# Kernel tuning notes

Measured on AMD Instinct MI355X. Metric: run time of the kernel, lower is better.

Reference implementation:

```python
import jax, jax.numpy as jnp
import numpy as np

B, T, NX, NXS, H, NY, NYS = 16384, 60, 4, 3, 64, 4, 3


def _lstm(x, h0, c0, Wih, Whh, bih, bhh):
    """PyTorch-convention LSTM (gate order i,f,g,o). x: [B,T,X]. Returns (hs [B,T,H], hT, cT)."""
    # precompute input contribution for all timesteps: [T,B,4H]
    xg = jnp.transpose(jnp.einsum('btx,gx->btg', x, Wih) + (bih + bhh), (1, 0, 2))

    def step(carry, xg_t):
        h, c = carry
        g = xg_t + h @ Whh.T
        i, f, gg, o = jnp.split(g, 4, axis=-1)
        c = jax.nn.sigmoid(f) * c + jax.nn.sigmoid(i) * jnp.tanh(gg)
        h = jax.nn.sigmoid(o) * jnp.tanh(c)
        return (h, c), h

    (hT, cT), hs = jax.lax.scan(step, (h0, c0), xg)
    return jnp.transpose(hs, (1, 0, 2)), hT, cT


def setup_inputs() -> dict:
    key = jax.random.key(0)
    ks = jax.random.split(key, 24)
    w = lambda k, shp: (jax.random.normal(k, shp, jnp.float32) * 0.1)
    return {
        'inputs_main': jax.random.normal(ks[0], (B, T, NX), jnp.float32),
        'inputs_aux': jax.random.normal(ks[1], (B, NXS), jnp.float32),
        'hx2': jax.random.normal(ks[2], (B, H), jnp.float32),
        'cx2': jax.random.normal(ks[3], (B, H), jnp.float32),
        'Ws1': w(ks[4], (H, NXS)), 'bs1': w(ks[5], (H,)),
        'Ws2': w(ks[6], (H, NXS)), 'bs2': w(ks[7], (H,)),
        'Wih1': w(ks[8], (4 * H, NX)), 'Whh1': w(ks[9], (4 * H, H)),
        'bih1': w(ks[10], (4 * H,)), 'bhh1': w(ks[11], (4 * H,)),
        'Wih2': w(ks[12], (4 * H, H)), 'Whh2': w(ks[13], (4 * H, H)),
        'bih2': w(ks[14], (4 * H,)), 'bhh2': w(ks[15], (4 * H,)),
        'Wlat': w(ks[16], (H, H)), 'blat': w(ks[17], (H,)),
        'Wout': w(ks[18], (NY, H)), 'bout': w(ks[19], (NY,)),
        'Wsfc': w(ks[20], (NYS, H)), 'bsfc': w(ks[21], (NYS,)),
    }


def reference(inputs_main, inputs_aux, hx2, cx2, Ws1, bs1, Ws2, bs2,
              Wih1, Whh1, bih1, bhh1, Wih2, Whh2, bih2, bhh2,
              Wlat, blat, Wout, bout, Wsfc, bsfc):
    # surface MLPs -> initial LSTM1 state (h raw, c tanh'd)
    hx = inputs_aux @ Ws1.T + bs1
    cx = jnp.tanh(inputs_aux @ Ws2.T + bs2)
    # run LSTM1 top-down (flipped levels)
    x1 = jnp.flip(inputs_main, axis=1)
    rnn1out, _, _ = _lstm(x1, hx, cx, Wih1, Whh1, bih1, bhh1)
    # flip back and run LSTM2 bottom-up with (hx2, cx2)
    # (the original calls rnn2 twice; only the second call's result is used)
    rnn1out_f = jnp.flip(rnn1out, axis=1)
    rnn2out, last_h, _ = _lstm(rnn1out_f, hx2, cx2, Wih2, Whh2, bih2, bhh2)
    # intermediate MLP + output head
    lat = rnn2out @ Wlat.T + blat                # [B,T,H]
    out = lat @ Wout.T + bout                    # [B,T,NY]
    out_sfc = jax.nn.relu(last_h @ Wsfc.T + bsfc)  # [B,NYS]
    return out, out_sfc
```

## Files before the change

### kernel.cpp

```cpp
#include <hip/hip_runtime.h>
#include <hip/hip_bf16.h>

#define BB 16384
#define TT 60

typedef short bf16x8 __attribute__((ext_vector_type(8)));
typedef float f32x4 __attribute__((ext_vector_type(4)));

__device__ __forceinline__ unsigned short f2bs(float f) {
    __hip_bfloat16 h = __float2bfloat16(f);
    return __builtin_bit_cast(unsigned short, h);
}

__device__ __forceinline__ unsigned cvtpk2(float lo, float hi) {
    unsigned r;
    asm("v_cvt_pk_bf16_f32 %0, %1, %2" : "=v"(r) : "v"(lo), "v"(hi));
    return r;
}

__device__ __forceinline__ void lstm_cell(float xi, float xf, float xg, float xo,
                                          float& c, float& h) {
    xi = __builtin_amdgcn_fmed3f(xi, -17.f, 17.f);
    xf = __builtin_amdgcn_fmed3f(xf, -17.f, 17.f);
    xo = __builtin_amdgcn_fmed3f(xo, -17.f, 17.f);
    xg = __builtin_amdgcn_fmed3f(xg, -11.f, 11.f);
    const float ei = __expf(-xi), ef = __expf(-xf), eo = __expf(-xo), eg = __expf(2.f * xg);
    const float di = 1.f + ei, df = 1.f + ef, dd = 1.f + eo, dg = 1.f + eg;
    const float a = di * df, b = dd * dg;
    const float R = __builtin_amdgcn_rcpf(a * b);
    const float si = df * b * R;
    const float sf = di * b * R;
    const float so = a * dg * R;
    const float tg = (eg - 1.f) * (a * dd) * R;
    const float cn = sf * c + si * tg;
    c = cn;
    const float tc = __builtin_amdgcn_fmed3f(cn, -11.f, 11.f);
    const float ec = __expf(2.f * tc);
    const float th = (ec - 1.f) * __builtin_amdgcn_rcpf(ec + 1.f);
    h = so * th;
}

#define STEP_BARRIER() do {                                   \
    asm volatile("s_waitcnt lgkmcnt(0)" ::: "memory");        \
    __builtin_amdgcn_s_barrier();                             \
    __builtin_amdgcn_sched_barrier(0);                        \
} while (0)

__device__ __forceinline__ bf16x8 pack8(float4 a, float4 b) {
    bf16x8 r;
    r[0] = (short)f2bs(a.x); r[1] = (short)f2bs(a.y);
    r[2] = (short)f2bs(a.z); r[3] = (short)f2bs(a.w);
    r[4] = (short)f2bs(b.x); r[5] = (short)f2bs(b.y);
    r[6] = (short)f2bs(b.z); r[7] = (short)f2bs(b.w);
    return r;
}

__global__ __launch_bounds__(256, 2) void k_fused(
    const float* __restrict__ xmain, const float* __restrict__ aux,
    const float* __restrict__ Ws1, const float* __restrict__ bs1,
    const float* __restrict__ Ws2, const float* __restrict__ bs2,
    const float* __restrict__ Wih1, const float* __restrict__ Whh1,
    const float* __restrict__ bih1, const float* __restrict__ bhh1,
    const float* __restrict__ hx2, const float* __restrict__ cx2,
    const float* __restrict__ Wih2, const float* __restrict__ Whh2,
    const float* __restrict__ bih2, const float* __restrict__ bhh2,
    const float* __restrict__ Wlat, const float* __restrict__ blat,
    const float* __restrict__ Wout, const float* __restrict__ bout,
    const float* __restrict__ Wsfc, const float* __restrict__ bsfc,
    unsigned short* __restrict__ rnn1t, float* __restrict__ out)
{
    __shared__ unsigned short hB[2 * 4096];
    __shared__ unsigned short whead[16 * 64];

    const int tid = threadIdx.x;
    {
        unsigned int* w32 = (unsigned int*)whead;
        w32[tid] = 0; w32[tid + 256] = 0;
    }
    const int hj = tid >> 6, lane = tid & 63;
    const int row16 = lane & 15, quad = lane >> 4;
    const int b0 = blockIdx.x * 32;
    const int swz = (row16 & 7) << 3;
    char* const hBb = (char*)hB;
    char* const whb = (char*)whead;

    const int j = hj * 16 + row16;
    const unsigned oA0 = (unsigned)(((row16 * 128 + 0 + quad * 8) ^ swz) * 2);
    const unsigned oA1 = (unsigned)(((row16 * 128 + 32 + quad * 8) ^ swz) * 2);
    const unsigned oA2 = (unsigned)(((row16 * 128 + 64 + quad * 8) ^ swz) * 2);
    const unsigned oA3 = (unsigned)(((row16 * 128 + 96 + quad * 8) ^ swz) * 2);
    unsigned oW[4];
    #pragma unroll
    for (int r = 0; r < 4; ++r) {
        const int m = quad * 4 + r;
        oW[r] = (unsigned)(((m * 128 + j) ^ ((m & 7) << 3)) * 2);
    }

    {
        {
            unsigned int* p32 = (unsigned int*)hB;
            #pragma unroll
            for (int e = 0; e < 16; ++e) p32[tid + 256 * e] = 0;
        }
        bf16x8 wf[4][3];
        float fb[4];
        #pragma unroll
        for (int i = 0; i < 4; ++i) {
            const int g = (hj + 4 * i) * 16 + row16;
            const float* wr = Whh1 + g * 64 + quad * 8;
            wf[i][0] = pack8(*(const float4*)wr, *(const float4*)(wr + 4));
            wf[i][1] = pack8(*(const float4*)(wr + 32), *(const float4*)(wr + 36));
            float4 z4 = {0.f, 0.f, 0.f, 0.f};
            float4 xw = z4;
            if (quad == 0) xw = *(const float4*)(Wih1 + g * 4);
            wf[i][2] = pack8(xw, z4);
            fb[i] = bih1[g] + bhh1[g];
        }
        __syncthreads();

        const unsigned oX = (unsigned)(((lane * 128 + 64) ^ ((lane & 7) << 3)) * 2);

        const float w10 = Ws1[j * 3], w11 = Ws1[j * 3 + 1], w12 = Ws1[j * 3 + 2], sb1v = bs1[j];
        const float w20 = Ws2[j * 3], w21 = Ws2[j * 3 + 1], w22 = Ws2[j * 3 + 2], sb2v = bs2[j];
        f32x4 cc[2];
        #pragma unroll
        for (int mh = 0; mh < 2; ++mh) {
            #pragma unroll
            for (int r = 0; r < 4; ++r) {
                const int m = mh * 16 + quad * 4 + r;
                const float a0v = aux[(b0 + m) * 3], a1v = aux[(b0 + m) * 3 + 1], a2v = aux[(b0 + m) * 3 + 2];
                float h0 = w10 * a0v + w11 * a1v + w12 * a2v + sb1v;
                float c0in = w20 * a0v + w21 * a1v + w22 * a2v + sb2v;
                c0in = __builtin_amdgcn_fmed3f(c0in, -11.f, 11.f);
                const float e0 = __expf(2.f * c0in);
                cc[mh][r] = (e0 - 1.f) * __builtin_amdgcn_rcpf(e0 + 1.f);
                *(unsigned short*)(hBb + oW[r] + mh * 4096) = f2bs(h0);
            }
        }
        if (hj == 2 && lane < 32) {
            float4 xv = ((const float4*)xmain)[(size_t)(b0 + lane) * TT + 59];
            uint2 p2 = { cvtpk2(xv.x, xv.y), cvtpk2(xv.z, xv.w) };
            *(uint2*)(hBb + oX) = p2;
        }
        __syncthreads();

        const float4* px = (const float4*)xmain + (size_t)(b0 + lane) * TT + 58;
        unsigned short* pst = rnn1t + ((size_t)60 * BB + b0 + ((hj >> 1) << 4) + row16) * 64 + ((hj & 1) << 5) + quad * 8;

        unsigned pofs = 0;
        #pragma unroll 1
        for (int s = 0; s < TT; ++s) {
            char* hbP = hBb + pofs;
            char* hbN = hBb + (pofs ^ 8192);
            float4 xv;
            if (hj == 2 && lane < 32 && s < TT - 1) xv = *px;
            bf16x8 a0[2], a1[2], a2[2];
            #pragma unroll
            for (int mh = 0; mh < 2; ++mh) {
                a0[mh] = *(const bf16x8*)(hbP + oA0 + mh * 4096);
                a1[mh] = *(const bf16x8*)(hbP + oA1 + mh * 4096);
                a2[mh] = *(const bf16x8*)(hbP + oA2 + mh * 4096);
            }
            if (s > 0) {
                bf16x8 sv = (hj == 0) ? a0[0] : (hj == 1) ? a1[0] : (hj == 2) ? a0[1] : a1[1];
                *(bf16x8*)pst = sv;
            }
            pst -= (size_t)BB * 64;
            px -= 1;

            f32x4 ac[2][4];
            #pragma unroll
            for (int mh = 0; mh < 2; ++mh)
                #pragma unroll
                for (int i = 0; i < 4; ++i) { f32x4 v = {fb[i], fb[i], fb[i], fb[i]}; ac[mh][i] = v; }
            #pragma unroll
            for (int mh = 0; mh < 2; ++mh) {
                #pragma unroll
                for (int i = 0; i < 4; ++i) {
                    ac[mh][i] = __builtin_amdgcn_mfma_f32_16x16x32_bf16(a0[mh], wf[i][0], ac[mh][i], 0, 0, 0);
                    ac[mh][i] = __builtin_amdgcn_mfma_f32_16x16x32_bf16(a1[mh], wf[i][1], ac[mh][i], 0, 0, 0);
                    ac[mh][i] = __builtin_amdgcn_mfma_f32_16x16x32_bf16(a2[mh], wf[i][2], ac[mh][i], 0, 0, 0);
                }
            }
            #pragma unroll
            for (int mh = 0; mh < 2; ++mh) {
                float hr[4];
                #pragma unroll
                for (int r = 0; r < 4; ++r) {
                    float cr = cc[mh][r];
                    lstm_cell(ac[mh][0][r], ac[mh][1][r], ac[mh][2][r], ac[mh][3][r], cr, hr[r]);
                    cc[mh][r] = cr;
                }
                const unsigned u01 = cvtpk2(hr[0], hr[1]);
                const unsigned u23 = cvtpk2(hr[2], hr[3]);
                *(unsigned short*)(hbN + oW[0] + mh * 4096) = (unsigned short)u01;
                *(unsigned short*)(hbN + oW[1] + mh * 4096) = (unsigned short)(u01 >> 16);
                *(unsigned short*)(hbN + oW[2] + mh * 4096) = (unsigned short)u23;
                *(unsigned short*)(hbN + oW[3] + mh * 4096) = (unsigned short)(u23 >> 16);
            }
            if (hj == 2 && lane < 32 && s < TT - 1) {
                uint2 p2 = { cvtpk2(xv.x, xv.y), cvtpk2(xv.z, xv.w) };
                *(uint2*)(hbN + oX) = p2;
            }
            STEP_BARRIER();
            pofs ^= 8192;
        }
        {
            char* hbP = hBb + pofs;
            bf16x8 sv;
            if (hj == 0)      sv = *(const bf16x8*)(hbP + oA0);
            else if (hj == 1) sv = *(const bf16x8*)(hbP + oA1);
            else if (hj == 2) sv = *(const bf16x8*)(hbP + oA0 + 4096);
            else              sv = *(const bf16x8*)(hbP + oA1 + 4096);
            *(bf16x8*)&rnn1t[((size_t)(b0 + ((hj >> 1) << 4) + row16)) * 64 + ((hj & 1) << 5) + quad * 8] = sv;
        }
    }

    __syncthreads();

    {
        bf16x8 wf[4][4];
        float fb[4];
        #pragma unroll
        for (int i = 0; i < 4; ++i) {
            const int g = (hj + 4 * i) * 16 + row16;
            const float* wh = Whh2 + g * 64 + quad * 8;
            const float* wi = Wih2 + g * 64 + quad * 8;
            wf[i][0] = pack8(*(const float4*)wh, *(const float4*)(wh + 4));
            wf[i][1] = pack8(*(const float4*)(wh + 32), *(const float4*)(wh + 36));
            wf[i][2] = pack8(*(const float4*)wi, *(const float4*)(wi + 4));
            wf[i][3] = pack8(*(const float4*)(wi + 32), *(const float4*)(wi + 36));
            fb[i] = bih2[g] + bhh2[g];
        }
        float bcomb = 0.f;
        if (row16 < 4) {
            float ss = 0.f;
            for (int jj = 0; jj < 64; ++jj) ss += Wout[row16 * 64 + jj] * blat[jj];
            bcomb = ss + bout[row16];
        } else if (row16 < 7) {
            bcomb = bsfc[row16 - 4];
        }
        {
            const int o = tid >> 6, k = tid & 63;
            float ss = 0.f;
            for (int jj = 0; jj < 64; ++jj) ss += Wout[o * 64 + jj] * Wlat[jj * 64 + k];
            whead[(o * 64 + k) ^ ((o & 7) << 3)] = f2bs(ss);
            if (tid < 192) {
                const int o2 = o + 4;
                whead[(o2 * 64 + k) ^ ((o2 & 7) << 3)] = f2bs(Wsfc[o * 64 + k]);
            }
        }

        const unsigned oPV = (unsigned)(((row16 * 128 + 64 + ((hj & 1) << 5) + quad * 8) ^ swz) * 2);
        const unsigned oH0 = (unsigned)(((row16 * 64 + 0 + quad * 8) ^ swz) * 2);
        const unsigned oH1 = (unsigned)(((row16 * 64 + 32 + quad * 8) ^ swz) * 2);

        f32x4 cc[2];
        #pragma unroll
        for (int mh = 0; mh < 2; ++mh) {
            #pragma unroll
            for (int r = 0; r < 4; ++r) {
                const int m = mh * 16 + quad * 4 + r;
                cc[mh][r] = cx2[(size_t)(b0 + m) * 64 + j];
                *(unsigned short*)(hBb + oW[r] + mh * 4096) = f2bs(hx2[(size_t)(b0 + m) * 64 + j]);
            }
        }
        if (hj < 2) {
            bf16x8 v0 = *(const bf16x8*)&rnn1t[((size_t)(b0 + row16)) * 64 + ((hj & 1) << 5) + quad * 8];
            bf16x8 v1 = *(const bf16x8*)&rnn1t[((size_t)(b0 + 16 + row16)) * 64 + ((hj & 1) << 5) + quad * 8];
            *(bf16x8*)(hBb + oPV) = v0;
            *(bf16x8*)(hBb + oPV + 4096) = v1;
        }
        __syncthreads();

        bf16x8 wh0 = *(const bf16x8*)(whb + oH0);
        bf16x8 wh1 = *(const bf16x8*)(whb + oH1);

        const unsigned short* ppv = rnn1t + ((size_t)BB + b0 + row16) * 64 + ((hj & 1) << 5) + quad * 8;
        float* po = out + ((size_t)(b0 + ((hj == 2) ? 16 : 0) + quad * 4) * TT) * 4 + row16;

        unsigned pofs = 0;
        #pragma unroll 1
        for (int t = 0; t < TT; ++t) {
            char* hbP = hBb + pofs;
            char* hbN = hBb + (pofs ^ 8192);
            bf16x8 pv0, pv1;
            if (hj < 2 && t < TT - 1) {
                pv0 = *(const bf16x8*)ppv;
                pv1 = *(const bf16x8*)(ppv + 16 * 64);
            }
            ppv += (size_t)BB * 64;

            bf16x8 a0[2], a1[2], a2[2], a3[2];
            #pragma unroll
            for (int mh = 0; mh < 2; ++mh) {
                a0[mh] = *(const bf16x8*)(hbP + oA0 + mh * 4096);
                a1[mh] = *(const bf16x8*)(hbP + oA1 + mh * 4096);
                a2[mh] = *(const bf16x8*)(hbP + oA2 + mh * 4096);
                a3[mh] = *(const bf16x8*)(hbP + oA3 + mh * 4096);
            }

            if (hj >= 2 && t > 0) {
                const bf16x8 ha0 = (hj == 3) ? a0[0] : a0[1];
                const bf16x8 ha1 = (hj == 3) ? a1[0] : a1[1];
                f32x4 hacc = {bcomb, bcomb, bcomb, bcomb};
                hacc = __builtin_amdgcn_mfma_f32_16x16x32_bf16(ha0, wh0, hacc, 0, 0, 0);
                hacc = __builtin_amdgcn_mfma_f32_16x16x32_bf16(ha1, wh1, hacc, 0, 0, 0);
                if (row16 < 4) {
                    #pragma unroll
                    for (int r = 0; r < 4; ++r)
                        po[r * TT * 4] = hacc[r];
                }
                po += 4;
            }

            f32x4 ac[2][4];
            #pragma unroll
            for (int mh = 0; mh < 2; ++mh)
                #pragma unroll
                for (int i = 0; i < 4; ++i) { f32x4 v = {fb[i], fb[i], fb[i], fb[i]}; ac[mh][i] = v; }
            #pragma unroll
            for (int mh = 0; mh < 2; ++mh) {
                #pragma unroll
                for (int i = 0; i < 4; ++i) {
                    ac[mh][i] = __builtin_amdgcn_mfma_f32_16x16x32_bf16(a0[mh], wf[i][0], ac[mh][i], 0, 0, 0);
                    ac[mh][i] = __builtin_amdgcn_mfma_f32_16x16x32_bf16(a1[mh], wf[i][1], ac[mh][i], 0, 0, 0);
                    ac[mh][i] = __builtin_amdgcn_mfma_f32_16x16x32_bf16(a2[mh], wf[i][2], ac[mh][i], 0, 0, 0);
                    ac[mh][i] = __builtin_amdgcn_mfma_f32_16x16x32_bf16(a3[mh], wf[i][3], ac[mh][i], 0, 0, 0);
                }
            }
            #pragma unroll
            for (int mh = 0; mh < 2; ++mh) {
                float hr[4];
                #pragma unroll
                for (int r = 0; r < 4; ++r) {
                    float cr = cc[mh][r];
                    lstm_cell(ac[mh][0][r], ac[mh][1][r], ac[mh][2][r], ac[mh][3][r], cr, hr[r]);
                    cc[mh][r] = cr;
                }
                const unsigned u01 = cvtpk2(hr[0], hr[1]);
                const unsigned u23 = cvtpk2(hr[2], hr[3]);
                *(unsigned short*)(hbN + oW[0] + mh * 4096) = (unsigned short)u01;
                *(unsigned short*)(hbN + oW[1] + mh * 4096) = (unsigned short)(u01 >> 16);
                *(unsigned short*)(hbN + oW[2] + mh * 4096) = (unsigned short)u23;
                *(unsigned short*)(hbN + oW[3] + mh * 4096) = (unsigned short)(u23 >> 16);
            }
            if (hj < 2 && t < TT - 1) {
                *(bf16x8*)(hbN + oPV) = pv0;
                *(bf16x8*)(hbN + oPV + 4096) = pv1;
            }
            STEP_BARRIER();
            pofs ^= 8192;
        }
        if (hj >= 2) {
            char* hbP = hBb + pofs;
            const int mho = (hj == 3) ? 0 : 4096;
            bf16x8 ea0 = *(const bf16x8*)(hbP + oA0 + mho);
            bf16x8 ea1 = *(const bf16x8*)(hbP + oA1 + mho);
            f32x4 hacc = {bcomb, bcomb, bcomb, bcomb};
            hacc = __builtin_amdgcn_mfma_f32_16x16x32_bf16(ea0, wh0, hacc, 0, 0, 0);
            hacc = __builtin_amdgcn_mfma_f32_16x16x32_bf16(ea1, wh1, hacc, 0, 0, 0);
            const int rb = b0 + ((hj == 2) ? 16 : 0) + quad * 4;
            if (row16 < 4) {
                #pragma unroll
                for (int r = 0; r < 4; ++r)
                    out[((size_t)(rb + r) * TT + 59) * 4 + row16] = hacc[r];
            } else if (row16 < 7) {
                float* osfc = out + (size_t)BB * TT * 4;
                #pragma unroll
                for (int r = 0; r < 4; ++r)
                    osfc[(size_t)(rb + r) * 3 + (row16 - 4)] = fmaxf(hacc[r], 0.f);
            }
        }
    }
}

extern "C" void kernel_launch(void* const* d_in, const int* in_sizes, int n_in,
                              void* d_out, int out_size, void* d_ws, size_t ws_size,
                              hipStream_t stream) {
    const float* xmain = (const float*)d_in[0];
    const float* aux   = (const float*)d_in[1];
    const float* hx2   = (const float*)d_in[2];
    const float* cx2   = (const float*)d_in[3];
    const float* Ws1   = (const float*)d_in[4];
    const float* bs1   = (const float*)d_in[5];
    const float* Ws2   = (const float*)d_in[6];
    const float* bs2   = (const float*)d_in[7];
    const float* Wih1  = (const float*)d_in[8];
    const float* Whh1  = (const float*)d_in[9];
    const float* bih1  = (const float*)d_in[10];
    const float* bhh1  = (const float*)d_in[11];
    const float* Wih2  = (const float*)d_in[12];
    const float* Whh2  = (const float*)d_in[13];
    const float* bih2  = (const float*)d_in[14];
    const float* bhh2  = (const float*)d_in[15];
    const float* Wlat  = (const float*)d_in[16];
    const float* blat  = (const float*)d_in[17];
    const float* Wout  = (const float*)d_in[18];
    const float* bout  = (const float*)d_in[19];
    const float* Wsfc  = (const float*)d_in[20];
    const float* bsfc  = (const float*)d_in[21];

    unsigned short* rnn1t = (unsigned short*)d_ws;
    float* out = (float*)d_out;

    dim3 grid(BB / 32), block(256);
    k_fused<<<grid, block, 0, stream>>>(xmain, aux, Ws1, bs1, Ws2, bs2,
                                        Wih1, Whh1, bih1, bhh1,
                                        hx2, cx2, Wih2, Whh2, bih2, bhh2,
                                        Wlat, blat, Wout, bout, Wsfc, bsfc,
                                        rnn1t, out);
}
```

Measured before the change: 232.9 us.

## Split batch halves across separate waves using 512-thread blocks

```diff
diff --git a/kernel.cpp b/kernel.cpp
--- a/kernel.cpp
+++ b/kernel.cpp
@@ -55,7 +55,7 @@
     return r;
 }
 
-__global__ __launch_bounds__(256, 2) void k_fused(
+__global__ __launch_bounds__(512, 4) void k_fused(
     const float* __restrict__ xmain, const float* __restrict__ aux,
     const float* __restrict__ Ws1, const float* __restrict__ bs1,
     const float* __restrict__ Ws2, const float* __restrict__ bs2,
@@ -73,14 +73,13 @@
     __shared__ unsigned short whead[16 * 64];
 
     const int tid = threadIdx.x;
-    {
-        unsigned int* w32 = (unsigned int*)whead;
-        w32[tid] = 0; w32[tid + 256] = 0;
-    }
-    const int hj = tid >> 6, lane = tid & 63;
+    ((unsigned int*)whead)[tid] = 0;
+    const int wv = tid >> 6, lane = tid & 63;
+    const int hj = wv & 3, mh = wv >> 2;
     const int row16 = lane & 15, quad = lane >> 4;
     const int b0 = blockIdx.x * 32;
     const int swz = (row16 & 7) << 3;
+    const int mo = mh * 4096;
     char* const hBb = (char*)hB;
     char* const whb = (char*)whead;
 
@@ -100,7 +99,7 @@
         {
             unsigned int* p32 = (unsigned int*)hB;
             #pragma unroll
-            for (int e = 0; e < 16; ++e) p32[tid + 256 * e] = 0;
+            for (int e = 0; e < 8; ++e) p32[tid + 512 * e] = 0;
         }
         bf16x8 wf[4][3];
         float fb[4];
@@ -122,22 +121,19 @@
 
         const float w10 = Ws1[j * 3], w11 = Ws1[j * 3 + 1], w12 = Ws1[j * 3 + 2], sb1v = bs1[j];
         const float w20 = Ws2[j * 3], w21 = Ws2[j * 3 + 1], w22 = Ws2[j * 3 + 2], sb2v = bs2[j];
-        f32x4 cc[2];
+        f32x4 cc;
         #pragma unroll
-        for (int mh = 0; mh < 2; ++mh) {
-            #pragma unroll
-            for (int r = 0; r < 4; ++r) {
-                const int m = mh * 16 + quad * 4 + r;
-                const float a0v = aux[(b0 + m) * 3], a1v = aux[(b0 + m) * 3 + 1], a2v = aux[(b0 + m) * 3 + 2];
-                float h0 = w10 * a0v + w11 * a1v + w12 * a2v + sb1v;
-                float c0in = w20 * a0v + w21 * a1v + w22 * a2v + sb2v;
-                c0in = __builtin_amdgcn_fmed3f(c0in, -11.f, 11.f);
-                const float e0 = __expf(2.f * c0in);
-                cc[mh][r] = (e0 - 1.f) * __builtin_amdgcn_rcpf(e0 + 1.f);
-                *(unsigned short*)(hBb + oW[r] + mh * 4096) = f2bs(h0);
-            }
-        }
-        if (hj == 2 && lane < 32) {
+        for (int r = 0; r < 4; ++r) {
+            const int m = mh * 16 + quad * 4 + r;
+            const float a0v = aux[(b0 + m) * 3], a1v = aux[(b0 + m) * 3 + 1], a2v = aux[(b0 + m) * 3 + 2];
+            float h0 = w10 * a0v + w11 * a1v + w12 * a2v + sb1v;
+            float c0in = w20 * a0v + w21 * a1v + w22 * a2v + sb2v;
+            c0in = __builtin_amdgcn_fmed3f(c0in, -11.f, 11.f);
+            const float e0 = __expf(2.f * c0in);
+            cc[r] = (e0 - 1.f) * __builtin_amdgcn_rcpf(e0 + 1.f);
+            *(unsigned short*)(hBb + oW[r] + mo) = f2bs(h0);
+        }
+        if (hj == 2 && mh == 0 && lane < 32) {
             float4 xv = ((const float4*)xmain)[(size_t)(b0 + lane) * TT + 59];
             uint2 p2 = { cvtpk2(xv.x, xv.y), cvtpk2(xv.z, xv.w) };
             *(uint2*)(hBb + oX) = p2;
@@ -145,7 +141,7 @@
         __syncthreads();
 
         const float4* px = (const float4*)xmain + (size_t)(b0 + lane) * TT + 58;
-        unsigned short* pst = rnn1t + ((size_t)60 * BB + b0 + ((hj >> 1) << 4) + row16) * 64 + ((hj & 1) << 5) + quad * 8;
+        unsigned short* pst = rnn1t + ((size_t)60 * BB + b0 + mh * 16 + row16) * 64 + hj * 32 + quad * 8;
 
         unsigned pofs = 0;
         #pragma unroll 1
@@ -153,66 +149,50 @@
             char* hbP = hBb + pofs;
             char* hbN = hBb + (pofs ^ 8192);
             float4 xv;
-            if (hj == 2 && lane < 32 && s < TT - 1) xv = *px;
-            bf16x8 a0[2], a1[2], a2[2];
-            #pragma unroll
-            for (int mh = 0; mh < 2; ++mh) {
-                a0[mh] = *(const bf16x8*)(hbP + oA0 + mh * 4096);
-                a1[mh] = *(const bf16x8*)(hbP + oA1 + mh * 4096);
-                a2[mh] = *(const bf16x8*)(hbP + oA2 + mh * 4096);
-            }
-            if (s > 0) {
-                bf16x8 sv = (hj == 0) ? a0[0] : (hj == 1) ? a1[0] : (hj == 2) ? a0[1] : a1[1];
-                *(bf16x8*)pst = sv;
+            if (hj == 2 && mh == 0 && lane < 32 && s < TT - 1) xv = *px;
+            bf16x8 a0 = *(const bf16x8*)(hbP + oA0 + mo);
+            bf16x8 a1 = *(const bf16x8*)(hbP + oA1 + mo);
+            bf16x8 a2 = *(const bf16x8*)(hbP + oA2 + mo);
+            if (s > 0 && hj < 2) {
+                *(bf16x8*)pst = (hj == 0) ? a0 : a1;
             }
             pst -= (size_t)BB * 64;
             px -= 1;
 
-            f32x4 ac[2][4];
-            #pragma unroll
-            for (int mh = 0; mh < 2; ++mh)
-                #pragma unroll
-                for (int i = 0; i < 4; ++i) { f32x4 v = {fb[i], fb[i], fb[i], fb[i]}; ac[mh][i] = v; }
-            #pragma unroll
-            for (int mh = 0; mh < 2; ++mh) {
-                #pragma unroll
-                for (int i = 0; i < 4; ++i) {
-                    ac[mh][i] = __builtin_amdgcn_mfma_f32_16x16x32_bf16(a0[mh], wf[i][0], ac[mh][i], 0, 0, 0);
-                    ac[mh][i] = __builtin_amdgcn_mfma_f32_16x16x32_bf16(a1[mh], wf[i][1], ac[mh][i], 0, 0, 0);
-                    ac[mh][i] = __builtin_amdgcn_mfma_f32_16x16x32_bf16(a2[mh], wf[i][2], ac[mh][i], 0, 0, 0);
-                }
-            }
-            #pragma unroll
-            for (int mh = 0; mh < 2; ++mh) {
-                float hr[4];
-                #pragma unroll
-                for (int r = 0; r < 4; ++r) {
-                    float cr = cc[mh][r];
-                    lstm_cell(ac[mh][0][r], ac[mh][1][r], ac[mh][2][r], ac[mh][3][r], cr, hr[r]);
-                    cc[mh][r] = cr;
-                }
-                const unsigned u01 = cvtpk2(hr[0], hr[1]);
-                const unsigned u23 = cvtpk2(hr[2], hr[3]);
-                *(unsigned short*)(hbN + oW[0] + mh * 4096) = (unsigned short)u01;
-                *(unsigned short*)(hbN + oW[1] + mh * 4096) = (unsigned short)(u01 >> 16);
-                *(unsigned short*)(hbN + oW[2] + mh * 4096) = (unsigned short)u23;
-                *(unsigned short*)(hbN + oW[3] + mh * 4096) = (unsigned short)(u23 >> 16);
-            }
-            if (hj == 2 && lane < 32 && s < TT - 1) {
+            f32x4 ac[4];
+            #pragma unroll
+            for (int i = 0; i < 4; ++i) { f32x4 v = {fb[i], fb[i], fb[i], fb[i]}; ac[i] = v; }
+            #pragma unroll
+            for (int i = 0; i < 4; ++i) {
+                ac[i] = __builtin_amdgcn_mfma_f32_16x16x32_bf16(a0, wf[i][0], ac[i], 0, 0, 0);
+                ac[i] = __builtin_amdgcn_mfma_f32_16x16x32_bf16(a1, wf[i][1], ac[i], 0, 0, 0);
+                ac[i] = __builtin_amdgcn_mfma_f32_16x16x32_bf16(a2, wf[i][2], ac[i], 0, 0, 0);
+            }
+            float hr[4];
+            #pragma unroll
+            for (int r = 0; r < 4; ++r) {
+                float cr = cc[r];
+                lstm_cell(ac[0][r], ac[1][r], ac[2][r], ac[3][r], cr, hr[r]);
+                cc[r] = cr;
+            }
+            const unsigned u01 = cvtpk2(hr[0], hr[1]);
+            const unsigned u23 = cvtpk2(hr[2], hr[3]);
+            *(unsigned short*)(hbN + oW[0] + mo) = (unsigned short)u01;
+            *(unsigned short*)(hbN + oW[1] + mo) = (unsigned short)(u01 >> 16);
+            *(unsigned short*)(hbN + oW[2] + mo) = (unsigned short)u23;
+            *(unsigned short*)(hbN + oW[3] + mo) = (unsigned short)(u23 >> 16);
+            if (hj == 2 && mh == 0 && lane < 32 && s < TT - 1) {
                 uint2 p2 = { cvtpk2(xv.x, xv.y), cvtpk2(xv.z, xv.w) };
                 *(uint2*)(hbN + oX) = p2;
             }
             STEP_BARRIER();
             pofs ^= 8192;
         }
-        {
+        if (hj < 2) {
             char* hbP = hBb + pofs;
-            bf16x8 sv;
-            if (hj == 0)      sv = *(const bf16x8*)(hbP + oA0);
-            else if (hj == 1) sv = *(const bf16x8*)(hbP + oA1);
-            else if (hj == 2) sv = *(const bf16x8*)(hbP + oA0 + 4096);
-            else              sv = *(const bf16x8*)(hbP + oA1 + 4096);
-            *(bf16x8*)&rnn1t[((size_t)(b0 + ((hj >> 1) << 4) + row16)) * 64 + ((hj & 1) << 5) + quad * 8] = sv;
+            bf16x8 sv = (hj == 0) ? *(const bf16x8*)(hbP + oA0 + mo)
+                                  : *(const bf16x8*)(hbP + oA1 + mo);
+            *(bf16x8*)&rnn1t[((size_t)(b0 + mh * 16 + row16)) * 64 + hj * 32 + quad * 8] = sv;
         }
     }
 
@@ -240,7 +220,7 @@
         } else if (row16 < 7) {
             bcomb = bsfc[row16 - 4];
         }
-        {
+        if (tid < 256) {
             const int o = tid >> 6, k = tid & 63;
             float ss = 0.f;
             for (int jj = 0; jj < 64; ++jj) ss += Wout[o * 64 + jj] * Wlat[jj * 64 + k];
@@ -251,61 +231,47 @@
             }
         }
 
-        const unsigned oPV = (unsigned)(((row16 * 128 + 64 + ((hj & 1) << 5) + quad * 8) ^ swz) * 2);
+        const unsigned oPV = (unsigned)(((row16 * 128 + 64 + hj * 32 + quad * 8) ^ swz) * 2);
         const unsigned oH0 = (unsigned)(((row16 * 64 + 0 + quad * 8) ^ swz) * 2);
         const unsigned oH1 = (unsigned)(((row16 * 64 + 32 + quad * 8) ^ swz) * 2);
 
-        f32x4 cc[2];
+        f32x4 cc;
         #pragma unroll
-        for (int mh = 0; mh < 2; ++mh) {
-            #pragma unroll
-            for (int r = 0; r < 4; ++r) {
-                const int m = mh * 16 + quad * 4 + r;
-                cc[mh][r] = cx2[(size_t)(b0 + m) * 64 + j];
-                *(unsigned short*)(hBb + oW[r] + mh * 4096) = f2bs(hx2[(size_t)(b0 + m) * 64 + j]);
-            }
+        for (int r = 0; r < 4; ++r) {
+            const int m = mh * 16 + quad * 4 + r;
+            cc[r] = cx2[(size_t)(b0 + m) * 64 + j];
+            *(unsigned short*)(hBb + oW[r] + mo) = f2bs(hx2[(size_t)(b0 + m) * 64 + j]);
         }
         if (hj < 2) {
-            bf16x8 v0 = *(const bf16x8*)&rnn1t[((size_t)(b0 + row16)) * 64 + ((hj & 1) << 5) + quad * 8];
-            bf16x8 v1 = *(const bf16x8*)&rnn1t[((size_t)(b0 + 16 + row16)) * 64 + ((hj & 1) << 5) + quad * 8];
-            *(bf16x8*)(hBb + oPV) = v0;
-            *(bf16x8*)(hBb + oPV + 4096) = v1;
+            bf16x8 v = *(const bf16x8*)&rnn1t[((size_t)(b0 + mh * 16 + row16)) * 64 + hj * 32 + quad * 8];
+            *(bf16x8*)(hBb + oPV + mo) = v;
         }
         __syncthreads();
 
         bf16x8 wh0 = *(const bf16x8*)(whb + oH0);
         bf16x8 wh1 = *(const bf16x8*)(whb + oH1);
 
-        const unsigned short* ppv = rnn1t + ((size_t)BB + b0 + row16) * 64 + ((hj & 1) << 5) + quad * 8;
-        float* po = out + ((size_t)(b0 + ((hj == 2) ? 16 : 0) + quad * 4) * TT) * 4 + row16;
+        const unsigned short* ppv = rnn1t + ((size_t)BB + b0 + mh * 16 + row16) * 64 + hj * 32 + quad * 8;
+        float* po = out + ((size_t)(b0 + mh * 16 + quad * 4) * TT) * 4 + row16;
 
         unsigned pofs = 0;
         #pragma unroll 1
         for (int t = 0; t < TT; ++t) {
             char* hbP = hBb + pofs;
             char* hbN = hBb + (pofs ^ 8192);
-            bf16x8 pv0, pv1;
-            if (hj < 2 && t < TT - 1) {
-                pv0 = *(const bf16x8*)ppv;
-                pv1 = *(const bf16x8*)(ppv + 16 * 64);
-            }
+            bf16x8 pv;
+            if (hj < 2 && t < TT - 1) pv = *(const bf16x8*)ppv;
             ppv += (size_t)BB * 64;
 
-            bf16x8 a0[2], a1[2], a2[2], a3[2];
-            #pragma unroll
-            for (int mh = 0; mh < 2; ++mh) {
-                a0[mh] = *(const bf16x8*)(hbP + oA0 + mh * 4096);
-                a1[mh] = *(const bf16x8*)(hbP + oA1 + mh * 4096);
-                a2[mh] = *(const bf16x8*)(hbP + oA2 + mh * 4096);
-                a3[mh] = *(const bf16x8*)(hbP + oA3 + mh * 4096);
-            }
-
-            if (hj >= 2 && t > 0) {
-                const bf16x8 ha0 = (hj == 3) ? a0[0] : a0[1];
-                const bf16x8 ha1 = (hj == 3) ? a1[0] : a1[1];
+            bf16x8 a0 = *(const bf16x8*)(hbP + oA0 + mo);
+            bf16x8 a1 = *(const bf16x8*)(hbP + oA1 + mo);
+            bf16x8 a2 = *(const bf16x8*)(hbP + oA2 + mo);
+            bf16x8 a3 = *(const bf16x8*)(hbP + oA3 + mo);
+
+            if (hj == 3 && t > 0) {
                 f32x4 hacc = {bcomb, bcomb, bcomb, bcomb};
-                hacc = __builtin_amdgcn_mfma_f32_16x16x32_bf16(ha0, wh0, hacc, 0, 0, 0);
-                hacc = __builtin_amdgcn_mfma_f32_16x16x32_bf16(ha1, wh1, hacc, 0, 0, 0);
+                hacc = __builtin_amdgcn_mfma_f32_16x16x32_bf16(a0, wh0, hacc, 0, 0, 0);
+                hacc = __builtin_amdgcn_mfma_f32_16x16x32_bf16(a1, wh1, hacc, 0, 0, 0);
                 if (row16 < 4) {
                     #pragma unroll
                     for (int r = 0; r < 4; ++r)
@@ -314,53 +280,41 @@
                 po += 4;
             }
 
-            f32x4 ac[2][4];
-            #pragma unroll
-            for (int mh = 0; mh < 2; ++mh)
-                #pragma unroll
-                for (int i = 0; i < 4; ++i) { f32x4 v = {fb[i], fb[i], fb[i], fb[i]}; ac[mh][i] = v; }
-            #pragma unroll
-            for (int mh = 0; mh < 2; ++mh) {
-                #pragma unroll
-                for (int i = 0; i < 4; ++i) {
-                    ac[mh][i] = __builtin_amdgcn_mfma_f32_16x16x32_bf16(a0[mh], wf[i][0], ac[mh][i], 0, 0, 0);
-                    ac[mh][i] = __builtin_amdgcn_mfma_f32_16x16x32_bf16(a1[mh], wf[i][1], ac[mh][i], 0, 0, 0);
-                    ac[mh][i] = __builtin_amdgcn_mfma_f32_16x16x32_bf16(a2[mh], wf[i][2], ac[mh][i], 0, 0, 0);
-                    ac[mh][i] = __builtin_amdgcn_mfma_f32_16x16x32_bf16(a3[mh], wf[i][3], ac[mh][i], 0, 0, 0);
-                }
-            }
-            #pragma unroll
-            for (int mh = 0; mh < 2; ++mh) {
-                float hr[4];
-                #pragma unroll
-                for (int r = 0; r < 4; ++r) {
-                    float cr = cc[mh][r];
-                    lstm_cell(ac[mh][0][r], ac[mh][1][r], ac[mh][2][r], ac[mh][3][r], cr, hr[r]);
-                    cc[mh][r] = cr;
-                }
-                const unsigned u01 = cvtpk2(hr[0], hr[1]);
-                const unsigned u23 = cvtpk2(hr[2], hr[3]);
-                *(unsigned short*)(hbN + oW[0] + mh * 4096) = (unsigned short)u01;
-                *(unsigned short*)(hbN + oW[1] + mh * 4096) = (unsigned short)(u01 >> 16);
-                *(unsigned short*)(hbN + oW[2] + mh * 4096) = (unsigned short)u23;
-                *(unsigned short*)(hbN + oW[3] + mh * 4096) = (unsigned short)(u23 >> 16);
-            }
-            if (hj < 2 && t < TT - 1) {
-                *(bf16x8*)(hbN + oPV) = pv0;
-                *(bf16x8*)(hbN + oPV + 4096) = pv1;
-            }
+            f32x4 ac[4];
+            #pragma unroll
+            for (int i = 0; i < 4; ++i) { f32x4 v = {fb[i], fb[i], fb[i], fb[i]}; ac[i] = v; }
+            #pragma unroll
+            for (int i = 0; i < 4; ++i) {
+                ac[i] = __builtin_amdgcn_mfma_f32_16x16x32_bf16(a0, wf[i][0], ac[i], 0, 0, 0);
+                ac[i] = __builtin_amdgcn_mfma_f32_16x16x32_bf16(a1, wf[i][1], ac[i], 0, 0, 0);
+                ac[i] = __builtin_amdgcn_mfma_f32_16x16x32_bf16(a2, wf[i][2], ac[i], 0, 0, 0);
+                ac[i] = __builtin_amdgcn_mfma_f32_16x16x32_bf16(a3, wf[i][3], ac[i], 0, 0, 0);
+            }
+            float hr[4];
+            #pragma unroll
+            for (int r = 0; r < 4; ++r) {
+                float cr = cc[r];
+                lstm_cell(ac[0][r], ac[1][r], ac[2][r], ac[3][r], cr, hr[r]);
+                cc[r] = cr;
+            }
+            const unsigned u01 = cvtpk2(hr[0], hr[1]);
+            const unsigned u23 = cvtpk2(hr[2], hr[3]);
+            *(unsigned short*)(hbN + oW[0] + mo) = (unsigned short)u01;
+            *(unsigned short*)(hbN + oW[1] + mo) = (unsigned short)(u01 >> 16);
+            *(unsigned short*)(hbN + oW[2] + mo) = (unsigned short)u23;
+            *(unsigned short*)(hbN + oW[3] + mo) = (unsigned short)(u23 >> 16);
+            if (hj < 2 && t < TT - 1) *(bf16x8*)(hbN + oPV + mo) = pv;
             STEP_BARRIER();
             pofs ^= 8192;
         }
-        if (hj >= 2) {
+        if (hj == 3) {
             char* hbP = hBb + pofs;
-            const int mho = (hj == 3) ? 0 : 4096;
-            bf16x8 ea0 = *(const bf16x8*)(hbP + oA0 + mho);
-            bf16x8 ea1 = *(const bf16x8*)(hbP + oA1 + mho);
+            bf16x8 ea0 = *(const bf16x8*)(hbP + oA0 + mo);
+            bf16x8 ea1 = *(const bf16x8*)(hbP + oA1 + mo);
             f32x4 hacc = {bcomb, bcomb, bcomb, bcomb};
             hacc = __builtin_amdgcn_mfma_f32_16x16x32_bf16(ea0, wh0, hacc, 0, 0, 0);
             hacc = __builtin_amdgcn_mfma_f32_16x16x32_bf16(ea1, wh1, hacc, 0, 0, 0);
-            const int rb = b0 + ((hj == 2) ? 16 : 0) + quad * 4;
+            const int rb = b0 + mh * 16 + quad * 4;
             if (row16 < 4) {
                 #pragma unroll
                 for (int r = 0; r < 4; ++r)
@@ -404,7 +358,7 @@
     unsigned short* rnn1t = (unsigned short*)d_ws;
     float* out = (float*)d_out;
 
-    dim3 grid(BB / 32), block(256);
+    dim3 grid(BB / 32), block(512);
     k_fused<<<grid, block, 0, stream>>>(xmain, aux, Ws1, bs1, Ws2, bs2,
                                         Wih1, Whh1, bih1, bhh1,
                                         hx2, cx2, Wih2, Whh2, bih2, bhh2,
```

After: 320.7 us. 1.38x slower.
